# Optimization experiments

Measured on AMD Instinct MI355X. Metric: run time of the kernel, lower is better.

The kernel has to match this reference:

```python
import jax, jax.numpy as jnp
import numpy as np


def setup_inputs() -> dict:
    key = jax.random.key(0)
    k1, k2 = jax.random.split(key)
    B, T, D, K = 16, 4096, 512, 2048
    x = jax.random.normal(k1, (B, T, D), dtype=jnp.float32)
    embed = jax.random.normal(k2, (K, D), dtype=jnp.float32)
    return {"x": x, "embed": embed}


def reference(x, embed):
    # encode: flatten to [N, D], nearest codebook entry by squared L2
    orig_shape = x.shape
    d = orig_shape[-1]
    flat = x.reshape(-1, d)  # [N, D]
    x_sq = jnp.sum(flat * flat, axis=1, keepdims=True)          # [N, 1]
    e_sq = jnp.sum(embed * embed, axis=1)[None, :]               # [1, K]
    dist = -(x_sq - 2.0 * (flat @ embed.T) + e_sq)               # [N, K]
    embed_ind = jnp.argmax(dist, axis=-1)                        # [N]
    embed_ind = embed_ind.reshape(orig_shape[:-1])               # [B, T]
    # decode: embedding gather
    quantize = embed[embed_ind]                                  # [B, T, D]
    return embed_ind, quantize
```

## Files before the change

### kernel.cpp

```cpp
#include <hip/hip_runtime.h>
#include <stdint.h>

#define DIM 512
#define BM  128
#define BK  128
#define DT  32
#define LDSX (BM + 4)

typedef __attribute__((ext_vector_type(8))) _Float16 f16x8;
typedef __attribute__((ext_vector_type(4))) _Float16 f16x4;
typedef __attribute__((ext_vector_type(4))) float f32x4;

__device__ __forceinline__ void async_cp16(const void* g, void* l) {
    __builtin_amdgcn_global_load_lds(
        (const __attribute__((address_space(1))) unsigned int*)g,
        (__attribute__((address_space(3))) unsigned int*)l, 16, 0, 0);
}

__global__ __launch_bounds__(256)
void esq_kernel(const float* __restrict__ embed, float* __restrict__ e_sq, int K) {
    int wave = (blockIdx.x * blockDim.x + threadIdx.x) >> 6;
    int lane = threadIdx.x & 63;
    if (wave >= K) return;
    const float* row = embed + (size_t)wave * DIM;
    float s = 0.f;
#pragma unroll
    for (int j = 0; j < DIM / 64; ++j) { float v = row[lane + 64 * j]; s += v * v; }
#pragma unroll
    for (int off = 32; off; off >>= 1) s += __shfl_down(s, off, 64);
    if (lane == 0) e_sq[wave] = s;
}

__global__ __launch_bounds__(256)
void cvt_f16_kernel(const float* __restrict__ src, _Float16* __restrict__ dst, int n4) {
    int i = blockIdx.x * 256 + threadIdx.x;
    if (i >= n4) return;
    float4 v = ((const float4*)src)[i];
    f16x4 h;
    h[0] = (_Float16)v.x; h[1] = (_Float16)v.y; h[2] = (_Float16)v.z; h[3] = (_Float16)v.w;
    ((f16x4*)dst)[i] = h;
}

template<int GV>
__device__ __forceinline__ void compute_group(const _Float16* ebuf,
    const f16x8 (&ah)[2][16], f32x4 (&acc)[2][4], int quad, int l15)
{
#pragma unroll
    for (int dtl = 0; dtl < 4; ++dtl) {
#pragma unroll
        for (int kwi = 0; kwi < 2; ++kwi) {
            const int pch = (kwi * 4 + quad) ^ (l15 & 7);
            f16x8 bh[4];
#pragma unroll
            for (int nt = 0; nt < 4; ++nt)
                bh[nt] = *(const f16x8*)(ebuf + dtl * 4096 + (nt * 16 + l15) * 64 + pch * 8);
#pragma unroll
            for (int mt = 0; mt < 2; ++mt)
#pragma unroll
                for (int nt = 0; nt < 4; ++nt)
                    acc[mt][nt] = __builtin_amdgcn_mfma_f32_16x16x32_f16(
                        ah[mt][(GV * 4 + dtl) * 2 + kwi], bh[nt], acc[mt][nt], 0, 0, 0);
        }
    }
}

__global__ __launch_bounds__(256, 2)
void vq_reg_kernel(const float* __restrict__ x, const _Float16* __restrict__ eh,
                   const float* __restrict__ e_sq, int* __restrict__ cand)
{
    __shared__ __align__(16) char smem[73728];
    _Float16* EB = (_Float16*)smem;
    const float* esq_l = (const float*)(smem + 65536);
    uint32_t* rk = (uint32_t*)smem;

    const int tid  = threadIdx.x;
    const int w    = tid >> 6, lane = tid & 63;
    const int quad = lane >> 4, l15 = lane & 15;
    const int r0   = blockIdx.x * 128;
    const int wrow = r0 + w * 32;

    uint32_t goff[8];
#pragma unroll
    for (int i = 0; i < 8; ++i) {
        const int s   = w * 512 + i * 64 + lane;
        const int dtl = s >> 9;
        const int rr  = (s >> 3) & 63;
        const int lch = (s & 7) ^ (rr & 7);
        goff[i] = (uint32_t)(rr * 512 + dtl * 64 + lch * 8);
    }

#pragma unroll
    for (int i = 0; i < 2; ++i) {
        const int sb = w * 128 + i * 64;
        async_cp16(e_sq + (size_t)(sb + lane) * 4, smem + 65536 + sb * 16);
    }
#pragma unroll
    for (int i = 0; i < 8; ++i)
        async_cp16(eh + goff[i], smem + (w * 512 + i * 64) * 16);

    f16x8 ah[2][16];
#pragma unroll
    for (int mt = 0; mt < 2; ++mt) {
        const float* xr = x + (size_t)(wrow + mt * 16 + l15) * DIM + quad * 8;
#pragma unroll
        for (int kw = 0; kw < 16; ++kw) {
            const float4 a0 = *(const float4*)(xr + kw * 32);
            const float4 a1 = *(const float4*)(xr + kw * 32 + 4);
            f16x8 h;
            h[0] = (_Float16)a0.x; h[1] = (_Float16)a0.y;
            h[2] = (_Float16)a0.z; h[3] = (_Float16)a0.w;
            h[4] = (_Float16)a1.x; h[5] = (_Float16)a1.y;
            h[6] = (_Float16)a1.z; h[7] = (_Float16)a1.w;
            ah[mt][kw] = h;
        }
    }

    uint32_t b1[8], b2[8];
#pragma unroll
    for (int i = 0; i < 8; ++i) { b1[i] = 0xFFFFFFFFu; b2[i] = 0xFFFFFFFFu; }

    __syncthreads();

    for (int kt = 0; kt < 32; ++kt) {
        f32x4 acc[2][4];
#pragma unroll
        for (int mt = 0; mt < 2; ++mt)
#pragma unroll
            for (int nt = 0; nt < 4; ++nt)
#pragma unroll
                for (int r = 0; r < 4; ++r) acc[mt][nt][r] = 0.f;

        const size_t kb = (size_t)kt * 32768;

#pragma unroll
        for (int i = 0; i < 8; ++i)
            async_cp16(eh + kb + 256 + goff[i], smem + 32768 + (w * 512 + i * 64) * 16);
        compute_group<0>(EB, ah, acc, quad, l15);
        __syncthreads();

        if (kt + 1 < 32) {
#pragma unroll
            for (int i = 0; i < 8; ++i)
                async_cp16(eh + kb + 32768 + goff[i], smem + (w * 512 + i * 64) * 16);
        }
        compute_group<1>(EB + 16384, ah, acc, quad, l15);
        __syncthreads();

#pragma unroll
        for (int nt = 0; nt < 4; ++nt) {
            const int c = kt * 64 + nt * 16 + l15;
            const float eqb = esq_l[c] + 1024.0f;
#pragma unroll
            for (int mt = 0; mt < 2; ++mt)
#pragma unroll
                for (int r = 0; r < 4; ++r) {
                    const float v = fmaf(-2.0f, acc[mt][nt][r], eqb);
                    const uint32_t u = (__float_as_uint(v) & 0xFFFFF800u) | (uint32_t)c;
                    const int s = mt * 4 + r;
                    const uint32_t mx = u > b1[s] ? u : b1[s];
                    b2[s] = mx < b2[s] ? mx : b2[s];
                    b1[s] = u < b1[s] ? u : b1[s];
                }
        }
    }

#pragma unroll
    for (int mt = 0; mt < 2; ++mt)
#pragma unroll
        for (int r = 0; r < 4; ++r) {
            const int row = w * 32 + mt * 16 + quad * 4 + r;
            const int s = mt * 4 + r;
            rk[row * 33 + l15 * 2]     = b1[s];
            rk[row * 33 + l15 * 2 + 1] = b2[s];
        }
    __syncthreads();
    if (tid < 128) {
        uint32_t t0 = 0xFFFFFFFFu, t1 = t0, t2 = t0, t3 = t0;
        for (int e = 0; e < 32; ++e) {
            const uint32_t u = rk[tid * 33 + e];
            if (u < t3) {
                if (u < t0)      { t3 = t2; t2 = t1; t1 = t0; t0 = u; }
                else if (u < t1) { t3 = t2; t2 = t1; t1 = u; }
                else if (u < t2) { t3 = t2; t2 = u; }
                else               t3 = u;
            }
        }
        const float v0 = __uint_as_float(t0 & 0xFFFFF800u);
        const float v1 = __uint_as_float(t1 & 0xFFFFF800u);
        uint32_t c0 = t0 & 2047u;
        if (!(v1 - v0 >= 1.0f)) c0 |= 0x80000000u;
        int4 c4;
        c4.x = (int)c0;
        c4.y = (int)(t1 & 2047u);
        c4.z = (int)(t2 & 2047u);
        c4.w = (int)(t3 & 2047u);
        *(int4*)(cand + (size_t)(r0 + tid) * 4) = c4;
    }
}

__global__ __launch_bounds__(256)
void verify_gather4_kernel(const float* __restrict__ x, const float* __restrict__ embed,
                           const float* __restrict__ e_sq, const int* __restrict__ cand,
                           float* __restrict__ out_idx, float* __restrict__ out_q) {
    const int w    = threadIdx.x >> 6;
    const int lane = threadIdx.x & 63;
    const int row0 = blockIdx.x * 16 + w * 4;
#pragma unroll
    for (int rr = 0; rr < 4; ++rr) {
        const int row = row0 + rr;
        const int4 cc = *(const int4*)(cand + (size_t)row * 4);
        f32x4* oq = (f32x4*)(out_q + (size_t)row * DIM);
        if (cc.x >= 0) {
            const f32x4* er = (const f32x4*)(embed + (size_t)cc.x * DIM);
            const f32x4 e0 = er[lane];
            const f32x4 e1 = er[lane + 64];
            __builtin_nontemporal_store(e0, oq + lane);
            __builtin_nontemporal_store(e1, oq + lane + 64);
            if (lane == 0) out_idx[row] = (float)cc.x;
        } else {
            const f32x4* xr = (const f32x4*)(x + (size_t)row * DIM);
            const f32x4 xv0 = __builtin_nontemporal_load(xr + lane);
            const f32x4 xv1 = __builtin_nontemporal_load(xr + lane + 64);
            const int cs[4] = {cc.x & 2047, cc.y & 2047, cc.z & 2047, cc.w & 2047};
            float best = 3.4e38f;
            int   bi   = 0x7fffffff;
            f32x4 g0 = {0.f, 0.f, 0.f, 0.f}, g1 = {0.f, 0.f, 0.f, 0.f};
#pragma unroll
            for (int k = 0; k < 4; ++k) {
                const int c = cs[k];
                const f32x4* er = (const f32x4*)(embed + (size_t)c * DIM);
                const f32x4 e0 = er[lane];
                const f32x4 e1 = er[lane + 64];
                float d = xv0[0] * e0[0] + xv0[1] * e0[1] + xv0[2] * e0[2] + xv0[3] * e0[3]
                        + xv1[0] * e1[0] + xv1[1] * e1[1] + xv1[2] * e1[2] + xv1[3] * e1[3];
#pragma unroll
                for (int off = 32; off; off >>= 1) d += __shfl_xor(d, off, 64);
                const float s = e_sq[c] - 2.0f * d;
                const bool better = (s < best) || (s == best && c < bi);
                best = better ? s : best;
                bi   = better ? c : bi;
                g0 = better ? e0 : g0;
                g1 = better ? e1 : g1;
            }
            if (lane == 0) out_idx[row] = (float)bi;
            __builtin_nontemporal_store(g0, oq + lane);
            __builtin_nontemporal_store(g1, oq + lane + 64);
        }
    }
}

__global__ __launch_bounds__(256)
void vq_argmin_kernel(const float* __restrict__ x, const float* __restrict__ embed,
                      const float* __restrict__ e_sq, float* __restrict__ out_idx,
                      int N, int K) {
    __shared__ float xs[DT * LDSX];
    __shared__ float es[DT * LDSX];
    __shared__ float sval[BM * 17];
    __shared__ int   sidx[BM * 17];
    const int tid = threadIdx.x;
    const int tx = tid & 15, ty = tid >> 4;
    const int r0 = blockIdx.x * BM;
    float best_val[8]; int best_idx[8];
#pragma unroll
    for (int i = 0; i < 8; ++i) { best_val[i] = 3.4e38f; best_idx[i] = 0; }
    const int nkt = K / BK;
    for (int kt = 0; kt < nkt; ++kt) {
        float acc[8][8];
#pragma unroll
        for (int i = 0; i < 8; ++i)
#pragma unroll
            for (int j = 0; j < 8; ++j) acc[i][j] = 0.f;
        for (int dt = 0; dt < DIM / DT; ++dt) {
            __syncthreads();
#pragma unroll
            for (int k = 0; k < 4; ++k) {
                int l = tid + k * 256, row = l >> 3, q = l & 7;
                const float4 v = *(const float4*)(x + (size_t)(r0 + row) * DIM + dt * DT + q * 4);
                xs[(q * 4 + 0) * LDSX + row] = v.x; xs[(q * 4 + 1) * LDSX + row] = v.y;
                xs[(q * 4 + 2) * LDSX + row] = v.z; xs[(q * 4 + 3) * LDSX + row] = v.w;
            }
#pragma unroll
            for (int k = 0; k < 4; ++k) {
                int l = tid + k * 256, row = l >> 3, q = l & 7;
                const float4 v = *(const float4*)(embed + (size_t)(kt * BK + row) * DIM + dt * DT + q * 4);
                es[(q * 4 + 0) * LDSX + row] = v.x; es[(q * 4 + 1) * LDSX + row] = v.y;
                es[(q * 4 + 2) * LDSX + row] = v.z; es[(q * 4 + 3) * LDSX + row] = v.w;
            }
            __syncthreads();
#pragma unroll
            for (int d = 0; d < DT; ++d) {
                const float4 a0 = *(const float4*)&xs[d * LDSX + 4 * ty];
                const float4 a1 = *(const float4*)&xs[d * LDSX + 4 * ty + 64];
                const float4 b0 = *(const float4*)&es[d * LDSX + 4 * tx];
                const float4 b1 = *(const float4*)&es[d * LDSX + 4 * tx + 64];
                const float a[8] = {a0.x, a0.y, a0.z, a0.w, a1.x, a1.y, a1.z, a1.w};
                const float b[8] = {b0.x, b0.y, b0.z, b0.w, b1.x, b1.y, b1.z, b1.w};
#pragma unroll
                for (int i = 0; i < 8; ++i)
#pragma unroll
                    for (int j = 0; j < 8; ++j) acc[i][j] += a[i] * b[j];
            }
        }
#pragma unroll
        for (int j = 0; j < 8; ++j) {
            const int c = kt * BK + 4 * tx + (j & 3) + 64 * (j >> 2);
            const float eq = e_sq[c];
#pragma unroll
            for (int i = 0; i < 8; ++i) {
                const float s = eq - 2.0f * acc[i][j];
                if (s < best_val[i]) { best_val[i] = s; best_idx[i] = c; }
            }
        }
    }
    __syncthreads();
#pragma unroll
    for (int i = 0; i < 8; ++i) {
        const int r = 4 * ty + (i & 3) + 64 * (i >> 2);
        sval[r * 17 + tx] = best_val[i]; sidx[r * 17 + tx] = best_idx[i];
    }
    __syncthreads();
    if (tid < BM) {
        float bv = sval[tid * 17 + 0]; int bi = sidx[tid * 17 + 0];
#pragma unroll
        for (int t = 1; t < 16; ++t) {
            const float v = sval[tid * 17 + t]; const int ix = sidx[tid * 17 + t];
            if (v < bv || (v == bv && ix < bi)) { bv = v; bi = ix; }
        }
        out_idx[r0 + tid] = (float)bi;
    }
}

__global__ __launch_bounds__(256)
void gather_kernel(const float* __restrict__ embed, const float* __restrict__ idx_f,
                   float* __restrict__ out_q) {
    const int row = blockIdx.x * 2 + (threadIdx.x >> 7);
    const int c = threadIdx.x & 127;
    const int idx = (int)idx_f[row];
    const float4 v = *(const float4*)(embed + (size_t)idx * DIM + c * 4);
    *(float4*)(out_q + (size_t)row * DIM + c * 4) = v;
}

extern "C" void kernel_launch(void* const* d_in, const int* in_sizes, int n_in,
                              void* d_out, int out_size, void* d_ws, size_t ws_size,
                              hipStream_t stream) {
    const float* x     = (const float*)d_in[0];
    const float* embed = (const float*)d_in[1];
    const int N = in_sizes[0] / DIM;
    const int K = in_sizes[1] / DIM;

    float* out_idx = (float*)d_out;
    float* out_q   = (float*)d_out + N;
    char* ws = (char*)d_ws;

    const size_t off_cand = 8192;
    const size_t off_eh   = off_cand + (size_t)N * 16;
    const size_t need     = off_eh + (size_t)K * DIM * 2;

    float* e_sq = (float*)ws;
    esq_kernel<<<(K + 3) / 4, 256, 0, stream>>>(embed, e_sq, K);

    if (ws_size >= need && K == 2048 && (N % 128) == 0) {
        _Float16* eh = (_Float16*)(ws + off_eh);
        int* cand = (int*)(ws + off_cand);
        cvt_f16_kernel<<<(K * DIM / 4 + 255) / 256, 256, 0, stream>>>(embed, eh, K * DIM / 4);
        vq_reg_kernel<<<N / 128, 256, 0, stream>>>(x, eh, e_sq, cand);
        verify_gather4_kernel<<<N / 16, 256, 0, stream>>>(x, embed, e_sq, cand, out_idx, out_q);
    } else {
        vq_argmin_kernel<<<N / BM, 256, 0, stream>>>(x, embed, e_sq, out_idx, N, K);
        gather_kernel<<<N / 2, 256, 0, stream>>>(embed, out_idx, out_q);
    }
}
```

Measured before the change: 357.8 us.

## Switch distance GEMM to 32x32x16 MFMA and split verify kernel per row

Replaces the 16x16x32 MFMA tiling with 32x32x16 f16 MFMA, so each wave holds a 32-row A fragment and two 32-column accumulators. This cuts LDS B-operand reads per FLOP, and the MFMA block is wrapped in s_setprio to favour matrix issue. The per-lane top-2 tracking grows to 16 slots and the final merge now scans 64 candidates per row. The verify/gather kernel drops from four rows per wave to one, launching four times more blocks for more parallelism. The cost is higher register pressure (32 A fragments plus 32 accumulators and 32 top-2 registers), which may hurt the 2-blocks-per-CU occupancy target.

```diff
diff --git a/kernel.cpp b/kernel.cpp
--- a/kernel.cpp
+++ b/kernel.cpp
@@ -10,6 +10,7 @@
 typedef __attribute__((ext_vector_type(8))) _Float16 f16x8;
 typedef __attribute__((ext_vector_type(4))) _Float16 f16x4;
 typedef __attribute__((ext_vector_type(4))) float f32x4;
+typedef __attribute__((ext_vector_type(16))) float f32x16;
 
 __device__ __forceinline__ void async_cp16(const void* g, void* l) {
     __builtin_amdgcn_global_load_lds(
@@ -43,24 +44,27 @@
 
 template<int GV>
 __device__ __forceinline__ void compute_group(const _Float16* ebuf,
-    const f16x8 (&ah)[2][16], f32x4 (&acc)[2][4], int quad, int l15)
+    const f16x8 (&ah)[32], f32x16 (&acc)[2], int c31, int h)
 {
+    const int sw = c31 & 7;
 #pragma unroll
     for (int dtl = 0; dtl < 4; ++dtl) {
-#pragma unroll
-        for (int kwi = 0; kwi < 2; ++kwi) {
-            const int pch = (kwi * 4 + quad) ^ (l15 & 7);
-            f16x8 bh[4];
-#pragma unroll
-            for (int nt = 0; nt < 4; ++nt)
-                bh[nt] = *(const f16x8*)(ebuf + dtl * 4096 + (nt * 16 + l15) * 64 + pch * 8);
-#pragma unroll
-            for (int mt = 0; mt < 2; ++mt)
-#pragma unroll
-                for (int nt = 0; nt < 4; ++nt)
-                    acc[mt][nt] = __builtin_amdgcn_mfma_f32_16x16x32_f16(
-                        ah[mt][(GV * 4 + dtl) * 2 + kwi], bh[nt], acc[mt][nt], 0, 0, 0);
-        }
+        f16x8 bh[4][2];
+#pragma unroll
+        for (int ks = 0; ks < 4; ++ks)
+#pragma unroll
+            for (int nt = 0; nt < 2; ++nt) {
+                const int chunk = (ks * 2 + h) ^ sw;
+                bh[ks][nt] = *(const f16x8*)(ebuf + dtl * 4096 + (nt * 32 + c31) * 64 + chunk * 8);
+            }
+        __builtin_amdgcn_s_setprio(1);
+#pragma unroll
+        for (int ks = 0; ks < 4; ++ks)
+#pragma unroll
+            for (int nt = 0; nt < 2; ++nt)
+                acc[nt] = __builtin_amdgcn_mfma_f32_32x32x16_f16(
+                    ah[GV * 16 + dtl * 4 + ks], bh[ks][nt], acc[nt], 0, 0, 0);
+        __builtin_amdgcn_s_setprio(0);
     }
 }
 
@@ -75,7 +79,7 @@
 
     const int tid  = threadIdx.x;
     const int w    = tid >> 6, lane = tid & 63;
-    const int quad = lane >> 4, l15 = lane & 15;
+    const int c31  = lane & 31, h = lane >> 5;
     const int r0   = blockIdx.x * 128;
     const int wrow = r0 + w * 32;
 
@@ -98,44 +102,41 @@
     for (int i = 0; i < 8; ++i)
         async_cp16(eh + goff[i], smem + (w * 512 + i * 64) * 16);
 
-    f16x8 ah[2][16];
-#pragma unroll
-    for (int mt = 0; mt < 2; ++mt) {
-        const float* xr = x + (size_t)(wrow + mt * 16 + l15) * DIM + quad * 8;
-#pragma unroll
-        for (int kw = 0; kw < 16; ++kw) {
-            const float4 a0 = *(const float4*)(xr + kw * 32);
-            const float4 a1 = *(const float4*)(xr + kw * 32 + 4);
-            f16x8 h;
-            h[0] = (_Float16)a0.x; h[1] = (_Float16)a0.y;
-            h[2] = (_Float16)a0.z; h[3] = (_Float16)a0.w;
-            h[4] = (_Float16)a1.x; h[5] = (_Float16)a1.y;
-            h[6] = (_Float16)a1.z; h[7] = (_Float16)a1.w;
-            ah[mt][kw] = h;
-        }
-    }
-
-    uint32_t b1[8], b2[8];
-#pragma unroll
-    for (int i = 0; i < 8; ++i) { b1[i] = 0xFFFFFFFFu; b2[i] = 0xFFFFFFFFu; }
+    f16x8 ah[32];
+    {
+        const float* xr = x + (size_t)(wrow + c31) * DIM + h * 8;
+#pragma unroll
+        for (int kw = 0; kw < 32; ++kw) {
+            const float4 a0 = *(const float4*)(xr + kw * 16);
+            const float4 a1 = *(const float4*)(xr + kw * 16 + 4);
+            f16x8 hh;
+            hh[0] = (_Float16)a0.x; hh[1] = (_Float16)a0.y;
+            hh[2] = (_Float16)a0.z; hh[3] = (_Float16)a0.w;
+            hh[4] = (_Float16)a1.x; hh[5] = (_Float16)a1.y;
+            hh[6] = (_Float16)a1.z; hh[7] = (_Float16)a1.w;
+            ah[kw] = hh;
+        }
+    }
+
+    uint32_t b1[16], b2[16];
+#pragma unroll
+    for (int i = 0; i < 16; ++i) { b1[i] = 0xFFFFFFFFu; b2[i] = 0xFFFFFFFFu; }
 
     __syncthreads();
 
     for (int kt = 0; kt < 32; ++kt) {
-        f32x4 acc[2][4];
-#pragma unroll
-        for (int mt = 0; mt < 2; ++mt)
-#pragma unroll
-            for (int nt = 0; nt < 4; ++nt)
-#pragma unroll
-                for (int r = 0; r < 4; ++r) acc[mt][nt][r] = 0.f;
+        f32x16 acc[2];
+#pragma unroll
+        for (int nt = 0; nt < 2; ++nt)
+#pragma unroll
+            for (int r = 0; r < 16; ++r) acc[nt][r] = 0.f;
 
         const size_t kb = (size_t)kt * 32768;
 
 #pragma unroll
         for (int i = 0; i < 8; ++i)
             async_cp16(eh + kb + 256 + goff[i], smem + 32768 + (w * 512 + i * 64) * 16);
-        compute_group<0>(EB, ah, acc, quad, l15);
+        compute_group<0>(EB, ah, acc, c31, h);
         __syncthreads();
 
         if (kt + 1 < 32) {
@@ -143,41 +144,36 @@
             for (int i = 0; i < 8; ++i)
                 async_cp16(eh + kb + 32768 + goff[i], smem + (w * 512 + i * 64) * 16);
         }
-        compute_group<1>(EB + 16384, ah, acc, quad, l15);
+        compute_group<1>(EB + 16384, ah, acc, c31, h);
         __syncthreads();
 
 #pragma unroll
-        for (int nt = 0; nt < 4; ++nt) {
-            const int c = kt * 64 + nt * 16 + l15;
+        for (int nt = 0; nt < 2; ++nt) {
+            const int c = kt * 64 + nt * 32 + c31;
             const float eqb = esq_l[c] + 1024.0f;
 #pragma unroll
-            for (int mt = 0; mt < 2; ++mt)
-#pragma unroll
-                for (int r = 0; r < 4; ++r) {
-                    const float v = fmaf(-2.0f, acc[mt][nt][r], eqb);
-                    const uint32_t u = (__float_as_uint(v) & 0xFFFFF800u) | (uint32_t)c;
-                    const int s = mt * 4 + r;
-                    const uint32_t mx = u > b1[s] ? u : b1[s];
-                    b2[s] = mx < b2[s] ? mx : b2[s];
-                    b1[s] = u < b1[s] ? u : b1[s];
-                }
-        }
-    }
-
-#pragma unroll
-    for (int mt = 0; mt < 2; ++mt)
-#pragma unroll
-        for (int r = 0; r < 4; ++r) {
-            const int row = w * 32 + mt * 16 + quad * 4 + r;
-            const int s = mt * 4 + r;
-            rk[row * 33 + l15 * 2]     = b1[s];
-            rk[row * 33 + l15 * 2 + 1] = b2[s];
-        }
+            for (int r = 0; r < 16; ++r) {
+                const float v = fmaf(-2.0f, acc[nt][r], eqb);
+                const uint32_t u = (__float_as_uint(v) & 0xFFFFF800u) | (uint32_t)c;
+                const uint32_t mx = u > b1[r] ? u : b1[r];
+                b2[r] = mx < b2[r] ? mx : b2[r];
+                b1[r] = u < b1[r] ? u : b1[r];
+            }
+        }
+    }
+
+    __syncthreads();
+#pragma unroll
+    for (int reg = 0; reg < 16; ++reg) {
+        const int row = w * 32 + (reg & 3) + 8 * (reg >> 2) + 4 * h;
+        rk[row * 65 + c31 * 2]     = b1[reg];
+        rk[row * 65 + c31 * 2 + 1] = b2[reg];
+    }
     __syncthreads();
     if (tid < 128) {
         uint32_t t0 = 0xFFFFFFFFu, t1 = t0, t2 = t0, t3 = t0;
-        for (int e = 0; e < 32; ++e) {
-            const uint32_t u = rk[tid * 33 + e];
+        for (int e = 0; e < 64; ++e) {
+            const uint32_t u = rk[tid * 65 + e];
             if (u < t3) {
                 if (u < t0)      { t3 = t2; t2 = t1; t1 = t0; t0 = u; }
                 else if (u < t1) { t3 = t2; t2 = t1; t1 = u; }
@@ -202,50 +198,45 @@
 void verify_gather4_kernel(const float* __restrict__ x, const float* __restrict__ embed,
                            const float* __restrict__ e_sq, const int* __restrict__ cand,
                            float* __restrict__ out_idx, float* __restrict__ out_q) {
-    const int w    = threadIdx.x >> 6;
+    const int row  = blockIdx.x * 4 + (threadIdx.x >> 6);
     const int lane = threadIdx.x & 63;
-    const int row0 = blockIdx.x * 16 + w * 4;
-#pragma unroll
-    for (int rr = 0; rr < 4; ++rr) {
-        const int row = row0 + rr;
-        const int4 cc = *(const int4*)(cand + (size_t)row * 4);
-        f32x4* oq = (f32x4*)(out_q + (size_t)row * DIM);
-        if (cc.x >= 0) {
-            const f32x4* er = (const f32x4*)(embed + (size_t)cc.x * DIM);
+    const int4 cc = *(const int4*)(cand + (size_t)row * 4);
+    f32x4* oq = (f32x4*)(out_q + (size_t)row * DIM);
+    if (cc.x >= 0) {
+        const f32x4* er = (const f32x4*)(embed + (size_t)cc.x * DIM);
+        const f32x4 e0 = er[lane];
+        const f32x4 e1 = er[lane + 64];
+        __builtin_nontemporal_store(e0, oq + lane);
+        __builtin_nontemporal_store(e1, oq + lane + 64);
+        if (lane == 0) out_idx[row] = (float)cc.x;
+    } else {
+        const f32x4* xr = (const f32x4*)(x + (size_t)row * DIM);
+        const f32x4 xv0 = __builtin_nontemporal_load(xr + lane);
+        const f32x4 xv1 = __builtin_nontemporal_load(xr + lane + 64);
+        const int cs[4] = {cc.x & 2047, cc.y & 2047, cc.z & 2047, cc.w & 2047};
+        float best = 3.4e38f;
+        int   bi   = 0x7fffffff;
+        f32x4 g0 = {0.f, 0.f, 0.f, 0.f}, g1 = {0.f, 0.f, 0.f, 0.f};
+#pragma unroll
+        for (int k = 0; k < 4; ++k) {
+            const int c = cs[k];
+            const f32x4* er = (const f32x4*)(embed + (size_t)c * DIM);
             const f32x4 e0 = er[lane];
             const f32x4 e1 = er[lane + 64];
-            __builtin_nontemporal_store(e0, oq + lane);
-            __builtin_nontemporal_store(e1, oq + lane + 64);
-            if (lane == 0) out_idx[row] = (float)cc.x;
-        } else {
-            const f32x4* xr = (const f32x4*)(x + (size_t)row * DIM);
-            const f32x4 xv0 = __builtin_nontemporal_load(xr + lane);
-            const f32x4 xv1 = __builtin_nontemporal_load(xr + lane + 64);
-            const int cs[4] = {cc.x & 2047, cc.y & 2047, cc.z & 2047, cc.w & 2047};
-            float best = 3.4e38f;
-            int   bi   = 0x7fffffff;
-            f32x4 g0 = {0.f, 0.f, 0.f, 0.f}, g1 = {0.f, 0.f, 0.f, 0.f};
-#pragma unroll
-            for (int k = 0; k < 4; ++k) {
-                const int c = cs[k];
-                const f32x4* er = (const f32x4*)(embed + (size_t)c * DIM);
-                const f32x4 e0 = er[lane];
-                const f32x4 e1 = er[lane + 64];
-                float d = xv0[0] * e0[0] + xv0[1] * e0[1] + xv0[2] * e0[2] + xv0[3] * e0[3]
-                        + xv1[0] * e1[0] + xv1[1] * e1[1] + xv1[2] * e1[2] + xv1[3] * e1[3];
-#pragma unroll
-                for (int off = 32; off; off >>= 1) d += __shfl_xor(d, off, 64);
-                const float s = e_sq[c] - 2.0f * d;
-                const bool better = (s < best) || (s == best && c < bi);
-                best = better ? s : best;
-                bi   = better ? c : bi;
-                g0 = better ? e0 : g0;
-                g1 = better ? e1 : g1;
-            }
-            if (lane == 0) out_idx[row] = (float)bi;
-            __builtin_nontemporal_store(g0, oq + lane);
-            __builtin_nontemporal_store(g1, oq + lane + 64);
-        }
+            float d = xv0[0] * e0[0] + xv0[1] * e0[1] + xv0[2] * e0[2] + xv0[3] * e0[3]
+                    + xv1[0] * e1[0] + xv1[1] * e1[1] + xv1[2] * e1[2] + xv1[3] * e1[3];
+#pragma unroll
+            for (int off = 32; off; off >>= 1) d += __shfl_xor(d, off, 64);
+            const float s = e_sq[c] - 2.0f * d;
+            const bool better = (s < best) || (s == best && c < bi);
+            best = better ? s : best;
+            bi   = better ? c : bi;
+            g0 = better ? e0 : g0;
+            g1 = better ? e1 : g1;
+        }
+        if (lane == 0) out_idx[row] = (float)bi;
+        __builtin_nontemporal_store(g0, oq + lane);
+        __builtin_nontemporal_store(g1, oq + lane + 64);
     }
 }
 
@@ -364,7 +355,7 @@
         int* cand = (int*)(ws + off_cand);
         cvt_f16_kernel<<<(K * DIM / 4 + 255) / 256, 256, 0, stream>>>(embed, eh, K * DIM / 4);
         vq_reg_kernel<<<N / 128, 256, 0, stream>>>(x, eh, e_sq, cand);
-        verify_gather4_kernel<<<N / 16, 256, 0, stream>>>(x, embed, e_sq, cand, out_idx, out_q);
+        verify_gather4_kernel<<<N / 4, 256, 0, stream>>>(x, embed, e_sq, cand, out_idx, out_q);
     } else {
         vq_argmin_kernel<<<N / BM, 256, 0, stream>>>(x, embed, e_sq, out_idx, N, K);
         gather_kernel<<<N / 2, 256, 0, stream>>>(embed, out_idx, out_q);
```

Result: slower. 401.1 us (+12.1%).
